# Optimization experiments

Hardware: AMD Instinct MI355X
Metric: run time of the kernel (lower is better)

The kernel has to match this reference:

```python
import jax, jax.numpy as jnp
import numpy as np

# The external iir2d op is a channel-wise separable 2D recursive IIR filter.
# Canonical reference semantics: first-order causal+anticausal recurrence applied
# along W then H:  y[t] = (1-a)*x[t] + a*y[t-1], with 'mirror' border handled by
# initializing the carry with the edge sample (y[0] = x[0]).
# filter_id selects the feedback coefficient a.
FID_TO_A = {1: 0.1, 3: 0.3, 4: 0.4, 8: 0.8}
FILTER_IDS = (1, 3, 4, 8)


def _iir_axis(x, a, axis):
    """Causal then anticausal first-order IIR along `axis` (mirror border)."""
    xm = jnp.moveaxis(x, axis, 0)

    def step(c, xt):
        y = (1.0 - a) * xt + a * c
        return y, y

    _, yf = jax.lax.scan(step, xm[0], xm)          # causal pass
    yr = yf[::-1]
    _, yb = jax.lax.scan(step, yr[0], yr)          # anticausal pass
    return jnp.moveaxis(yb[::-1], 0, axis)


def _iir2d_nhwc(x, a):
    # Channel-wise separable 2D IIR: along W (axis 2) then H (axis 1).
    return _iir_axis(_iir_axis(x, a, 2), a, 1)


def setup_inputs() -> dict:
    key = jax.random.key(0)
    kx, kg = jax.random.split(key)
    N, H, W, C = 4, 256, 256, 96
    x = jax.random.normal(kx, (N, H, W, C), dtype=jnp.float32)
    gate_logits = jax.random.normal(kg, (len(FILTER_IDS), C), dtype=jnp.float32)
    return {"x": x, "gate_logits": gate_logits}


def reference(x, gate_logits):
    # softmax over the filter axis, broadcast as (F,1,1,1,C)
    weights = jax.nn.softmax(gate_logits, axis=0).reshape(
        (len(FILTER_IDS), 1, 1, 1, -1))
    ys = [_iir2d_nhwc(x, FID_TO_A[fid]) for fid in FILTER_IDS]
    stacked = jnp.stack(ys, axis=0)               # (F, N, H, W, C)
    return jnp.sum(stacked * weights, axis=0)      # (N, H, W, C)
```

## Files before the change

kernel.cpp:

```cpp
#include <hip/hip_runtime.h>
#include <hip/hip_fp16.h>

#define N_ 4
#define H_ 256
#define W_ 256
#define C_ 96
#define CH 48
#define NC4 12
#define TP 258
#define SP 132
#define NFILT 4

__constant__ float c_a[NFILT] = {0.1f, 0.3f, 0.4f, 0.8f};

__device__ __forceinline__ void scan_fwd(float &v0, float &v1, float &v2, float &v3,
                                         float a, int lane) {
  const float b = 1.0f - a;
  const float a2 = a * a, a3 = a2 * a, a4 = a2 * a2;
  float t0 = b * v0;
  float t1 = fmaf(a, t0, b * v1);
  float t2 = fmaf(a, t1, b * v2);
  float t3 = fmaf(a, t2, b * v3);
  if (lane == 0) {
    t0 = fmaf(a,  v0, t0);
    t1 = fmaf(a2, v0, t1);
    t2 = fmaf(a3, v0, t2);
    t3 = fmaf(a4, v0, t3);
  }
  float c = t3;
  float m = a4;
  #pragma unroll
  for (int d = 1; d <= 8; d <<= 1) {
    float o = __shfl_up(c, (unsigned)d, 64);
    if (lane >= d) c = fmaf(m, o, c);
    m = m * m;
  }
  float cin = __shfl_up(c, 1u, 64);
  if (lane == 0) cin = 0.0f;
  v0 = fmaf(a,  cin, t0);
  v1 = fmaf(a2, cin, t1);
  v2 = fmaf(a3, cin, t2);
  v3 = fmaf(a4, cin, t3);
}

__device__ __forceinline__ void scan_bwd(float &v0, float &v1, float &v2, float &v3,
                                         float a, int lane) {
  const float b = 1.0f - a;
  const float a2 = a * a, a3 = a2 * a, a4 = a2 * a2;
  float t3 = b * v3;
  float t2 = fmaf(a, t3, b * v2);
  float t1 = fmaf(a, t2, b * v1);
  float t0 = fmaf(a, t1, b * v0);
  if (lane == 63) {
    t3 = fmaf(a,  v3, t3);
    t2 = fmaf(a2, v3, t2);
    t1 = fmaf(a3, v3, t1);
    t0 = fmaf(a4, v3, t0);
  }
  float c = t0;
  float m = a4;
  #pragma unroll
  for (int d = 1; d <= 8; d <<= 1) {
    float o = __shfl_down(c, (unsigned)d, 64);
    if (lane < 64 - d) c = fmaf(m, o, c);
    m = m * m;
  }
  float cin = __shfl_down(c, 1u, 64);
  if (lane == 63) cin = 0.0f;
  v3 = fmaf(a,  cin, t3);
  v2 = fmaf(a2, cin, t2);
  v1 = fmaf(a3, cin, t1);
  v0 = fmaf(a4, cin, t0);
}

__global__ __launch_bounds__(256, 4)
void k_wpass(const float* __restrict__ x, __half* __restrict__ inter,
             int f_start, int nf) {
  __shared__ __half tile[CH * TP];
  const int chalf = blockIdx.x & 1;
  const int fi    = blockIdx.x >> 1;
  const int row   = blockIdx.y;
  const int h     = row & 255;
  const int c0    = chalf * CH;
  const float a   = c_a[f_start + fi];
  const int t     = threadIdx.x;
  const int wave  = t >> 6, lane = t & 63;

  const float* xrow = x + (size_t)row * (W_ * C_) + c0;
  #pragma unroll
  for (int i = 0; i < 12; ++i) {
    int idx = t + i * 256;
    int w = idx / NC4, c4 = idx % NC4;
    const float4 v = *(const float4*)(xrow + (size_t)w * C_ + 4 * c4);
    tile[(4 * c4 + 0) * TP + w] = __float2half(v.x);
    tile[(4 * c4 + 1) * TP + w] = __float2half(v.y);
    tile[(4 * c4 + 2) * TP + w] = __float2half(v.z);
    tile[(4 * c4 + 3) * TP + w] = __float2half(v.w);
  }
  __syncthreads();
  #pragma unroll
  for (int ci = 0; ci < NC4; ++ci) {
    const int c = wave + 4 * ci;
    __half2* p = (__half2*)(tile + c * TP + 4 * lane);
    float2 f01 = __half22float2(p[0]);
    float2 f23 = __half22float2(p[1]);
    float v0 = f01.x, v1 = f01.y, v2 = f23.x, v3 = f23.y;
    scan_fwd(v0, v1, v2, v3, a, lane);
    scan_bwd(v0, v1, v2, v3, a, lane);
    p[0] = __floats2half2_rn(v0, v1);
    p[1] = __floats2half2_rn(v2, v3);
  }
  __syncthreads();
  __half* ibase = inter + (((size_t)(fi * 2 + chalf) * N_ * W_ + (size_t)(row >> 8) * W_)
                           * (H_ * CH)) + (size_t)h * CH;
  #pragma unroll
  for (int i = 0; i < 6; ++i) {
    int idx = t + i * 256;
    int w = idx / 6, j = idx % 6;
    union { uint4 u; ushort s[8]; } pk;
    #pragma unroll
    for (int k = 0; k < 8; ++k)
      pk.s[k] = __half_as_ushort(tile[(8 * j + k) * TP + w]);
    *(uint4*)(ibase + (size_t)w * (H_ * CH) + 8 * j) = pk.u;
  }
}

__global__ __launch_bounds__(256, 4)
void k_hpass(const __half* __restrict__ inter, const float* __restrict__ gate,
             float* __restrict__ out, int f_start, int nf, int accumulate) {
  __shared__ __align__(16) unsigned char smem[CH * SP * 4];
  __half* tile = (__half*)smem;
  float*  stage = (float*)smem;
  __shared__ float wlds[NFILT * CH];
  const int chalf = blockIdx.x;
  const int col   = blockIdx.y;
  const int n = col >> 8, w = col & 255;
  const int c0 = chalf * CH;
  const int t = threadIdx.x;
  const int wave = t >> 6, lane = t & 63;

  if (t < CH) {
    const int c = c0 + t;
    float g0 = gate[0 * C_ + c], g1 = gate[1 * C_ + c];
    float g2 = gate[2 * C_ + c], g3 = gate[3 * C_ + c];
    float mx = fmaxf(fmaxf(g0, g1), fmaxf(g2, g3));
    float e0 = __expf(g0 - mx), e1 = __expf(g1 - mx);
    float e2 = __expf(g2 - mx), e3 = __expf(g3 - mx);
    float inv = 1.0f / (e0 + e1 + e2 + e3);
    wlds[0 * CH + t] = e0 * inv;
    wlds[1 * CH + t] = e1 * inv;
    wlds[2 * CH + t] = e2 * inv;
    wlds[3 * CH + t] = e3 * inv;
  }

  float acc[NC4][4];
  #pragma unroll
  for (int ci = 0; ci < NC4; ++ci)
    acc[ci][0] = acc[ci][1] = acc[ci][2] = acc[ci][3] = 0.0f;

  const size_t chunk = (size_t)H_ * CH;
  uint4 pf[6];
  {
    const uint4* src = (const uint4*)(inter +
        ((size_t)(0 * 2 + chalf) * N_ * W_ + (size_t)n * W_ + w) * chunk);
    #pragma unroll
    for (int i = 0; i < 6; ++i) pf[i] = src[i * 256 + t];
  }

  for (int fi = 0; fi < nf; ++fi) {
    __syncthreads();
    #pragma unroll
    for (int i = 0; i < 6; ++i) {
      int e = i * 256 + t;
      int h = e / 6, c8 = e % 6;
      union { uint4 u; ushort s[8]; } pk;
      pk.u = pf[i];
      #pragma unroll
      for (int k = 0; k < 8; ++k)
        tile[(8 * c8 + k) * TP + h] = __ushort_as_half(pk.s[k]);
    }
    __syncthreads();
    if (fi + 1 < nf) {
      const uint4* src = (const uint4*)(inter +
          ((size_t)((fi + 1) * 2 + chalf) * N_ * W_ + (size_t)n * W_ + w) * chunk);
      #pragma unroll
      for (int i = 0; i < 6; ++i) pf[i] = src[i * 256 + t];
    }
    const float a = c_a[f_start + fi];
    #pragma unroll
    for (int ci = 0; ci < NC4; ++ci) {
      const int c = wave + 4 * ci;
      const __half2* p = (const __half2*)(tile + c * TP + 4 * lane);
      float2 f01 = __half22float2(p[0]);
      float2 f23 = __half22float2(p[1]);
      float v0 = f01.x, v1 = f01.y, v2 = f23.x, v3 = f23.y;
      scan_fwd(v0, v1, v2, v3, a, lane);
      scan_bwd(v0, v1, v2, v3, a, lane);
      const float wg = wlds[(f_start + fi) * CH + c];
      acc[ci][0] = fmaf(wg, v0, acc[ci][0]);
      acc[ci][1] = fmaf(wg, v1, acc[ci][1]);
      acc[ci][2] = fmaf(wg, v2, acc[ci][2]);
      acc[ci][3] = fmaf(wg, v3, acc[ci][3]);
    }
  }

  #pragma unroll
  for (int r = 0; r < 2; ++r) {
    __syncthreads();
    if ((lane >> 5) == r) {
      const int hl = 4 * (lane & 31);
      #pragma unroll
      for (int ci = 0; ci < NC4; ++ci) {
        float4* sp = (float4*)(stage + (wave + 4 * ci) * SP + hl);
        *sp = make_float4(acc[ci][0], acc[ci][1], acc[ci][2], acc[ci][3]);
      }
    }
    __syncthreads();
    float* obase = out + (((size_t)n * H_ + 128 * r) * W_ + w) * C_ + c0;
    #pragma unroll
    for (int i = 0; i < 6; ++i) {
      int idx = t + i * 256;
      int hl = idx / NC4, c4 = idx % NC4;
      float4 v;
      v.x = stage[(4 * c4 + 0) * SP + hl];
      v.y = stage[(4 * c4 + 1) * SP + hl];
      v.z = stage[(4 * c4 + 2) * SP + hl];
      v.w = stage[(4 * c4 + 3) * SP + hl];
      float4* dst = (float4*)(obase + (size_t)hl * (W_ * C_) + 4 * c4);
      if (accumulate) {
        float4 pv = *dst;
        v.x += pv.x; v.y += pv.y; v.z += pv.z; v.w += pv.w;
      }
      *dst = v;
    }
  }
}

extern "C" void kernel_launch(void* const* d_in, const int* in_sizes, int n_in,
                              void* d_out, int out_size, void* d_ws, size_t ws_size,
                              hipStream_t stream) {
  const float* x    = (const float*)d_in[0];
  const float* gate = (const float*)d_in[1];
  float* out        = (float*)d_out;
  __half* inter     = (__half*)d_ws;

  const size_t per_f = (size_t)N_ * H_ * W_ * C_ * sizeof(__half);
  int batch = 1;
  if (ws_size >= 4 * per_f)      batch = 4;
  else if (ws_size >= 2 * per_f) batch = 2;

  int done = 0;
  while (done < NFILT) {
    int nf = NFILT - done;
    if (nf > batch) nf = batch;
    dim3 g1(2 * nf, N_ * H_);
    k_wpass<<<g1, dim3(256), 0, stream>>>(x, inter, done, nf);
    dim3 g2(2, N_ * W_);
    k_hpass<<<g2, dim3(256), 0, stream>>>(inter, gate, out, done, nf,
                                          done > 0 ? 1 : 0);
    done += nf;
  }
}
```

Baseline: 339.6 us.

## Fuse W and H passes into one cooperative kernel with grid sync

Adds a cooperative kernel that runs the W-pass and the H-pass in one launch of 1024 persistent blocks separated by a grid-wide sync, with a fallback to the two-kernel path if the cooperative launch fails. Each block handles one row and then one column and loops over filters and channel halves serially. This removes one kernel launch and its gap, but cuts parallelism from 8192 blocks to 1024 per phase, so latency hiding depends on 4 blocks per CU fitting at once, and the grid sync adds a barrier cost.

```diff
diff --git a/kernel.cpp b/kernel.cpp
--- a/kernel.cpp
+++ b/kernel.cpp
@@ -1,12 +1,15 @@
 #include <hip/hip_runtime.h>
 #include <hip/hip_fp16.h>
+#include <hip/hip_cooperative_groups.h>
+
+namespace cg = cooperative_groups;
 
 #define N_ 4
 #define H_ 256
 #define W_ 256
 #define C_ 96
 #define CH 48
-#define NC4 12
+#define NFR 12
 #define TP 258
 #define SP 132
 #define NFILT 4
@@ -74,6 +77,173 @@
 }
 
 __global__ __launch_bounds__(256, 4)
+void k_fused(const float* __restrict__ x, const float* __restrict__ gate,
+             float* __restrict__ out, __half* __restrict__ inter,
+             int f_start, int nf, int accumulate) {
+  __shared__ __align__(16) unsigned char smem[CH * SP * 4];
+  __half* tile  = (__half*)smem;
+  float*  stage = (float*)smem;
+  __shared__ float wlds[NFILT * C_];
+  const int b    = blockIdx.x;
+  const int t    = threadIdx.x;
+  const int wave = t >> 6, lane = t & 63;
+
+  if (t < C_) {
+    float g0 = gate[0 * C_ + t], g1 = gate[1 * C_ + t];
+    float g2 = gate[2 * C_ + t], g3 = gate[3 * C_ + t];
+    float mx = fmaxf(fmaxf(g0, g1), fmaxf(g2, g3));
+    float e0 = __expf(g0 - mx), e1 = __expf(g1 - mx);
+    float e2 = __expf(g2 - mx), e3 = __expf(g3 - mx);
+    float inv = 1.0f / (e0 + e1 + e2 + e3);
+    wlds[0 * C_ + t] = e0 * inv;
+    wlds[1 * C_ + t] = e1 * inv;
+    wlds[2 * C_ + t] = e2 * inv;
+    wlds[3 * C_ + t] = e3 * inv;
+  }
+
+  {
+    const int row = b;
+    const int h = row & 255, n = row >> 8;
+    for (int k = 0; k < 2 * nf; ++k) {
+      const int chalf = k / nf, fi = k % nf;
+      const float a = c_a[f_start + fi];
+      const int c0 = chalf * CH;
+      const float* xrow = x + (size_t)row * (W_ * C_) + c0;
+      #pragma unroll
+      for (int i = 0; i < 12; ++i) {
+        int idx = t + i * 256;
+        int w = idx / 12, c4 = idx % 12;
+        const float4 v = *(const float4*)(xrow + (size_t)w * C_ + 4 * c4);
+        tile[(4 * c4 + 0) * TP + w] = __float2half(v.x);
+        tile[(4 * c4 + 1) * TP + w] = __float2half(v.y);
+        tile[(4 * c4 + 2) * TP + w] = __float2half(v.z);
+        tile[(4 * c4 + 3) * TP + w] = __float2half(v.w);
+      }
+      __syncthreads();
+      #pragma unroll
+      for (int ci = 0; ci < NFR; ++ci) {
+        const int c = wave + 4 * ci;
+        __half2* p = (__half2*)(tile + c * TP + 4 * lane);
+        float2 f01 = __half22float2(p[0]);
+        float2 f23 = __half22float2(p[1]);
+        float v0 = f01.x, v1 = f01.y, v2 = f23.x, v3 = f23.y;
+        scan_fwd(v0, v1, v2, v3, a, lane);
+        scan_bwd(v0, v1, v2, v3, a, lane);
+        p[0] = __floats2half2_rn(v0, v1);
+        p[1] = __floats2half2_rn(v2, v3);
+      }
+      __syncthreads();
+      __half* ibase = inter + (((size_t)(fi * 2 + chalf) * N_ * W_
+                                + (size_t)n * W_) * (H_ * CH)) + (size_t)h * CH;
+      #pragma unroll
+      for (int i = 0; i < 6; ++i) {
+        int idx = t + i * 256;
+        int w = idx / 6, j = idx % 6;
+        union { uint4 u; ushort s[8]; } pk;
+        #pragma unroll
+        for (int kk = 0; kk < 8; ++kk)
+          pk.s[kk] = __half_as_ushort(tile[(8 * j + kk) * TP + w]);
+        *(uint4*)(ibase + (size_t)w * (H_ * CH) + 8 * j) = pk.u;
+      }
+      if (k + 1 < 2 * nf) __syncthreads();
+    }
+  }
+
+  __threadfence();
+  cg::this_grid().sync();
+
+  {
+    const int col = b;
+    const int n = col >> 8, w = col & 255;
+    const size_t chunk = (size_t)H_ * CH;
+    for (int k = 0; k < 2; ++k) {
+      const int chalf = k;
+      const int c0 = chalf * CH;
+      float acc[NFR][4];
+      #pragma unroll
+      for (int ci = 0; ci < NFR; ++ci)
+        acc[ci][0] = acc[ci][1] = acc[ci][2] = acc[ci][3] = 0.0f;
+
+      uint4 pf[6];
+      {
+        const uint4* src = (const uint4*)(inter +
+            ((size_t)(0 * 2 + chalf) * N_ * W_ + (size_t)n * W_ + w) * chunk);
+        #pragma unroll
+        for (int i = 0; i < 6; ++i) pf[i] = src[i * 256 + t];
+      }
+
+      for (int fi = 0; fi < nf; ++fi) {
+        __syncthreads();
+        #pragma unroll
+        for (int i = 0; i < 6; ++i) {
+          int e = i * 256 + t;
+          int hh = e / 6, c8 = e % 6;
+          union { uint4 u; ushort s[8]; } pk;
+          pk.u = pf[i];
+          #pragma unroll
+          for (int kk = 0; kk < 8; ++kk)
+            tile[(8 * c8 + kk) * TP + hh] = __ushort_as_half(pk.s[kk]);
+        }
+        __syncthreads();
+        if (fi + 1 < nf) {
+          const uint4* src = (const uint4*)(inter +
+              ((size_t)((fi + 1) * 2 + chalf) * N_ * W_ + (size_t)n * W_ + w) * chunk);
+          #pragma unroll
+          for (int i = 0; i < 6; ++i) pf[i] = src[i * 256 + t];
+        }
+        const float a = c_a[f_start + fi];
+        #pragma unroll
+        for (int ci = 0; ci < NFR; ++ci) {
+          const int c = wave + 4 * ci;
+          const __half2* p = (const __half2*)(tile + c * TP + 4 * lane);
+          float2 f01 = __half22float2(p[0]);
+          float2 f23 = __half22float2(p[1]);
+          float v0 = f01.x, v1 = f01.y, v2 = f23.x, v3 = f23.y;
+          scan_fwd(v0, v1, v2, v3, a, lane);
+          scan_bwd(v0, v1, v2, v3, a, lane);
+          const float wg = wlds[(f_start + fi) * C_ + c0 + c];
+          acc[ci][0] = fmaf(wg, v0, acc[ci][0]);
+          acc[ci][1] = fmaf(wg, v1, acc[ci][1]);
+          acc[ci][2] = fmaf(wg, v2, acc[ci][2]);
+          acc[ci][3] = fmaf(wg, v3, acc[ci][3]);
+        }
+      }
+
+      #pragma unroll
+      for (int r = 0; r < 2; ++r) {
+        __syncthreads();
+        if ((lane >> 5) == r) {
+          const int hl = 4 * (lane & 31);
+          #pragma unroll
+          for (int ci = 0; ci < NFR; ++ci) {
+            float4* sp = (float4*)(stage + (wave + 4 * ci) * SP + hl);
+            *sp = make_float4(acc[ci][0], acc[ci][1], acc[ci][2], acc[ci][3]);
+          }
+        }
+        __syncthreads();
+        float* obase = out + (((size_t)n * H_ + 128 * r) * W_ + w) * C_ + c0;
+        #pragma unroll
+        for (int i = 0; i < 6; ++i) {
+          int idx = t + i * 256;
+          int hl = idx / 12, c4 = idx % 12;
+          float4 v;
+          v.x = stage[(4 * c4 + 0) * SP + hl];
+          v.y = stage[(4 * c4 + 1) * SP + hl];
+          v.z = stage[(4 * c4 + 2) * SP + hl];
+          v.w = stage[(4 * c4 + 3) * SP + hl];
+          float4* dst = (float4*)(obase + (size_t)hl * (W_ * C_) + 4 * c4);
+          if (accumulate) {
+            float4 pv = *dst;
+            v.x += pv.x; v.y += pv.y; v.z += pv.z; v.w += pv.w;
+          }
+          *dst = v;
+        }
+      }
+    }
+  }
+}
+
+__global__ __launch_bounds__(256, 4)
 void k_wpass(const float* __restrict__ x, __half* __restrict__ inter,
              int f_start, int nf) {
   __shared__ __half tile[CH * TP];
@@ -90,7 +260,7 @@
   #pragma unroll
   for (int i = 0; i < 12; ++i) {
     int idx = t + i * 256;
-    int w = idx / NC4, c4 = idx % NC4;
+    int w = idx / 12, c4 = idx % 12;
     const float4 v = *(const float4*)(xrow + (size_t)w * C_ + 4 * c4);
     tile[(4 * c4 + 0) * TP + w] = __float2half(v.x);
     tile[(4 * c4 + 1) * TP + w] = __float2half(v.y);
@@ -99,7 +269,7 @@
   }
   __syncthreads();
   #pragma unroll
-  for (int ci = 0; ci < NC4; ++ci) {
+  for (int ci = 0; ci < NFR; ++ci) {
     const int c = wave + 4 * ci;
     __half2* p = (__half2*)(tile + c * TP + 4 * lane);
     float2 f01 = __half22float2(p[0]);
@@ -119,8 +289,8 @@
     int w = idx / 6, j = idx % 6;
     union { uint4 u; ushort s[8]; } pk;
     #pragma unroll
-    for (int k = 0; k < 8; ++k)
-      pk.s[k] = __half_as_ushort(tile[(8 * j + k) * TP + w]);
+    for (int kk = 0; kk < 8; ++kk)
+      pk.s[kk] = __half_as_ushort(tile[(8 * j + kk) * TP + w]);
     *(uint4*)(ibase + (size_t)w * (H_ * CH) + 8 * j) = pk.u;
   }
 }
@@ -153,9 +323,9 @@
     wlds[3 * CH + t] = e3 * inv;
   }
 
-  float acc[NC4][4];
-  #pragma unroll
-  for (int ci = 0; ci < NC4; ++ci)
+  float acc[NFR][4];
+  #pragma unroll
+  for (int ci = 0; ci < NFR; ++ci)
     acc[ci][0] = acc[ci][1] = acc[ci][2] = acc[ci][3] = 0.0f;
 
   const size_t chunk = (size_t)H_ * CH;
@@ -172,12 +342,12 @@
     #pragma unroll
     for (int i = 0; i < 6; ++i) {
       int e = i * 256 + t;
-      int h = e / 6, c8 = e % 6;
+      int hh = e / 6, c8 = e % 6;
       union { uint4 u; ushort s[8]; } pk;
       pk.u = pf[i];
       #pragma unroll
-      for (int k = 0; k < 8; ++k)
-        tile[(8 * c8 + k) * TP + h] = __ushort_as_half(pk.s[k]);
+      for (int kk = 0; kk < 8; ++kk)
+        tile[(8 * c8 + kk) * TP + hh] = __ushort_as_half(pk.s[kk]);
     }
     __syncthreads();
     if (fi + 1 < nf) {
@@ -188,7 +358,7 @@
     }
     const float a = c_a[f_start + fi];
     #pragma unroll
-    for (int ci = 0; ci < NC4; ++ci) {
+    for (int ci = 0; ci < NFR; ++ci) {
       const int c = wave + 4 * ci;
       const __half2* p = (const __half2*)(tile + c * TP + 4 * lane);
       float2 f01 = __half22float2(p[0]);
@@ -210,7 +380,7 @@
     if ((lane >> 5) == r) {
       const int hl = 4 * (lane & 31);
       #pragma unroll
-      for (int ci = 0; ci < NC4; ++ci) {
+      for (int ci = 0; ci < NFR; ++ci) {
         float4* sp = (float4*)(stage + (wave + 4 * ci) * SP + hl);
         *sp = make_float4(acc[ci][0], acc[ci][1], acc[ci][2], acc[ci][3]);
       }
@@ -220,7 +390,7 @@
     #pragma unroll
     for (int i = 0; i < 6; ++i) {
       int idx = t + i * 256;
-      int hl = idx / NC4, c4 = idx % NC4;
+      int hl = idx / 12, c4 = idx % 12;
       float4 v;
       v.x = stage[(4 * c4 + 0) * SP + hl];
       v.y = stage[(4 * c4 + 1) * SP + hl];
@@ -249,15 +419,33 @@
   if (ws_size >= 4 * per_f)      batch = 4;
   else if (ws_size >= 2 * per_f) batch = 2;
 
+  bool coop_ok = true;
   int done = 0;
   while (done < NFILT) {
     int nf = NFILT - done;
     if (nf > batch) nf = batch;
-    dim3 g1(2 * nf, N_ * H_);
-    k_wpass<<<g1, dim3(256), 0, stream>>>(x, inter, done, nf);
-    dim3 g2(2, N_ * W_);
-    k_hpass<<<g2, dim3(256), 0, stream>>>(inter, gate, out, done, nf,
-                                          done > 0 ? 1 : 0);
+    int f_start = done;
+    int acc = done > 0 ? 1 : 0;
+    bool launched = false;
+    if (coop_ok) {
+      void* args[] = {(void*)&x, (void*)&gate, (void*)&out, (void*)&inter,
+                      (void*)&f_start, (void*)&nf, (void*)&acc};
+      hipError_t e = hipLaunchCooperativeKernel((const void*)k_fused,
+                                                dim3(1024), dim3(256),
+                                                args, 0, stream);
+      if (e == hipSuccess) {
+        launched = true;
+      } else {
+        (void)hipGetLastError();
+        coop_ok = false;
+      }
+    }
+    if (!launched) {
+      dim3 g1(2 * nf, N_ * H_);
+      k_wpass<<<g1, dim3(256), 0, stream>>>(x, inter, f_start, nf);
+      dim3 g2(2, N_ * W_);
+      k_hpass<<<g2, dim3(256), 0, stream>>>(inter, gate, out, f_start, nf, acc);
+    }
     done += nf;
   }
 }
```

Measured after the change: 657.0 us. 93.4% more time.
